# Kernel tuning notes

Hardware: AMD Instinct MI355X
Metric: run time of the kernel (lower is better)

## Reference

```python
import jax, jax.numpy as jnp
import numpy as np

NUM_CLASSES = 10
EPS = 1e-6


def setup_inputs() -> dict:
    key = jax.random.key(0)
    kx, ky, k1, k2, k3, k4 = jax.random.split(key, 6)
    B, N, F = 64, 4096, 256
    hidden, out_dim = 64, 128
    return {
        "X_support": jax.random.normal(kx, (B, N, F), dtype=jnp.float32),
        "y_support": jax.random.randint(ky, (B, N), 0, NUM_CLASSES, dtype=jnp.int64),
        "W1": jax.random.normal(k1, (6, hidden), dtype=jnp.float32) * 0.4,
        "b1": jax.random.normal(k2, (hidden,), dtype=jnp.float32) * 0.02,
        "W2": jax.random.normal(k3, (hidden, out_dim), dtype=jnp.float32) * 0.12,
        "b2": jax.random.normal(k4, (out_dim,), dtype=jnp.float32) * 0.02,
    }


def _stats(X, y):
    # X: [B, N, F] float, y: [B, N] int labels in [0, NUM_CLASSES)
    B, N, F = X.shape
    missing_rate = jnp.isnan(X).astype(jnp.float32).mean(axis=1)        # [B, F]
    cleaned = jnp.nan_to_num(X, nan=0.0)                                # [B, N, F]

    # unique ratio per column: count distinct via sorted adjacent diffs
    srt = jnp.sort(cleaned, axis=1)
    uniq = 1.0 + (jnp.diff(srt, axis=1) != 0).astype(jnp.float32).sum(axis=1)  # [B, F]
    unique_ratio = uniq / max(1, N)

    mean = cleaned.mean(axis=1)                                         # [B, F]
    variance = cleaned.var(axis=1)                                      # [B, F] (unbiased=False)
    mean_abs = jnp.abs(cleaned).mean(axis=1)
    max_abs = jnp.abs(cleaned).max(axis=1)

    # classification target score: between-class variance / overall variance
    onehot = jax.nn.one_hot(y, NUM_CLASSES, dtype=jnp.float32)          # [B, N, C]
    counts = onehot.sum(axis=1)                                         # [B, C]
    class_sums = jnp.einsum("bnc,bnf->bcf", onehot, cleaned)            # [B, C, F]
    class_means = class_sums / jnp.maximum(counts, 1.0)[:, :, None]     # [B, C, F] (0 for empty class)
    dev2 = jnp.square(class_means - mean[:, None, :])                   # [B, C, F]
    between_var = jnp.einsum("bc,bcf->bf", counts, dev2) / jnp.maximum(counts.sum(axis=1), 1.0)[:, None]
    overall_var = jnp.maximum(variance, EPS)
    target_score = between_var / overall_var                            # [B, F]

    stats = jnp.stack(
        [target_score, missing_rate, unique_ratio, variance, mean_abs, max_abs], axis=-1
    )  # [B, F, 6]
    return jnp.nan_to_num(stats, nan=0.0, posinf=0.0, neginf=0.0)


def reference(X_support, y_support, W1, b1, W2, b2):
    stats = _stats(X_support, y_support)                                # [B, F, 6]
    h = jax.nn.gelu(stats @ W1 + b1, approximate=False)
    return h @ W2 + b2                                                  # [B, F, output_dim]
```

## Files before the change

### kernel.cpp

```cpp
#include <hip/hip_runtime.h>
#include <math.h>

#define NB 64
#define NN 4096
#define NF 256
#define NC 10
#define NSPLIT 16
#define CH 256
#define LW 263
#define EMPTYK 0xFFFFFFFFu

__global__ void k_counts(const int* __restrict__ Y, int* __restrict__ counts) {
  __shared__ int hist[NC];
  const int b = blockIdx.x;
  if (threadIdx.x < NC) hist[threadIdx.x] = 0;
  __syncthreads();
  for (int i = threadIdx.x; i < NN; i += blockDim.x) {
    int c = Y[b * NN + i];
    if (c >= 0 && c < NC) atomicAdd(&hist[c], 1);
  }
  __syncthreads();
  if (threadIdx.x < NC) counts[b * NC + threadIdx.x] = hist[threadIdx.x];
}

__global__ __launch_bounds__(256) void k_stats(const float* __restrict__ X,
                                               const int* __restrict__ Y,
                                               unsigned* __restrict__ XT,
                                               float* __restrict__ P) {
  __shared__ unsigned ldsT[32 * LW];
  const int bi = blockIdx.x;
  const int b = bi >> 4, sp = bi & 15;
  const int t = threadIdx.x;
  const int w = t >> 6, l = t & 63;
  const int n0 = sp * CH;
  const float4* Xv = (const float4*)X;

  float s1[4] = {0, 0, 0, 0}, s2[4] = {0, 0, 0, 0}, sab[4] = {0, 0, 0, 0};
  float mab[4] = {0, 0, 0, 0}, nanc[4] = {0, 0, 0, 0};
  float cls[NC][4] = {};
  const int colbase = 4 * l + (l >> 3);

#define ADD4(c) do { cls[c][0]+=cv[0]; cls[c][1]+=cv[1]; cls[c][2]+=cv[2]; cls[c][3]+=cv[3]; } while(0)

  for (int tile = 0; tile < CH / 32; ++tile) {
#pragma unroll 4
    for (int it = 0; it < 8; ++it) {
      const int r = it * 4 + w;
      const int n = n0 + tile * 32 + r;
      float4 v4 = Xv[(size_t)(b * NN + n) * (NF / 4) + l];
      float v[4] = {v4.x, v4.y, v4.z, v4.w};
      float cv[4];
      unsigned ub[4];
#pragma unroll
      for (int q = 0; q < 4; ++q) {
        float c = v[q];
        if (c != c) { nanc[q] += 1.f; c = 0.f; }
        cv[q] = c;
        s1[q] += c;
        s2[q] = fmaf(c, c, s2[q]);
        float a = fabsf(c);
        sab[q] += a;
        mab[q] = fmaxf(mab[q], a);
        ub[q] = (c == 0.f) ? 0u : __float_as_uint(c);
      }
      const int ys = __builtin_amdgcn_readfirstlane(Y[b * NN + n]);
      switch (ys) {
        case 0: ADD4(0); break; case 1: ADD4(1); break;
        case 2: ADD4(2); break; case 3: ADD4(3); break;
        case 4: ADD4(4); break; case 5: ADD4(5); break;
        case 6: ADD4(6); break; case 7: ADD4(7); break;
        case 8: ADD4(8); break; case 9: ADD4(9); break;
        default: break;
      }
      const int lb = r * LW + colbase;
      ldsT[lb + 0] = ub[0]; ldsT[lb + 1] = ub[1];
      ldsT[lb + 2] = ub[2]; ldsT[lb + 3] = ub[3];
    }
    __syncthreads();
#pragma unroll
    for (int j = 0; j < 8; ++j) {
      const int idx = t + 256 * j;
      const int f = idx >> 3, rr4 = idx & 7;
      const int fo = f + (f >> 5);
      uint4 o;
      o.x = ldsT[(rr4 * 4 + 0) * LW + fo];
      o.y = ldsT[(rr4 * 4 + 1) * LW + fo];
      o.z = ldsT[(rr4 * 4 + 2) * LW + fo];
      o.w = ldsT[(rr4 * 4 + 3) * LW + fo];
      ((uint4*)(XT + (size_t)(b * NF + f) * NN + n0 + tile * 32))[rr4] = o;
    }
    __syncthreads();
  }

  float* red = (float*)ldsT;
  for (int ph = 0; ph < 4; ++ph) {
    if (w == ph) {
#pragma unroll
      for (int ff = 0; ff < 4; ++ff) {
        const int f = 4 * l + ff;
        float vals[16];
        vals[0] = s1[ff]; vals[1] = s2[ff]; vals[2] = sab[ff];
        vals[3] = mab[ff]; vals[4] = nanc[ff];
#pragma unroll
        for (int c = 0; c < NC; ++c) vals[5 + c] = cls[c][ff];
        vals[15] = 0.f;
        if (ph == 0) {
#pragma unroll
          for (int s = 0; s < 16; ++s) red[f * 16 + s] = vals[s];
        } else {
          red[f * 16 + 0] += vals[0];
          red[f * 16 + 1] += vals[1];
          red[f * 16 + 2] += vals[2];
          red[f * 16 + 3] = fmaxf(red[f * 16 + 3], vals[3]);
          red[f * 16 + 4] += vals[4];
#pragma unroll
          for (int c = 0; c < NC; ++c) red[f * 16 + 5 + c] += vals[5 + c];
        }
      }
    }
    __syncthreads();
  }
  float4* Pv = (float4*)(P + ((size_t)(b * NSPLIT + sp) * NF + t) * 16);
  const float4* rv = (const float4*)(red + t * 16);
  Pv[0] = rv[0]; Pv[1] = rv[1]; Pv[2] = rv[2]; Pv[3] = rv[3];
#undef ADD4
}

__global__ __launch_bounds__(256) void k_uniq(const unsigned* __restrict__ XT,
                                              unsigned* __restrict__ uniq) {
  __shared__ unsigned tab[8192];
  const int t = threadIdx.x;
  const size_t base = (size_t)blockIdx.x * NN;

  const uint4* Xv = (const uint4*)(XT + base);
  uint4 kv0 = Xv[t], kv1 = Xv[256 + t], kv2 = Xv[512 + t], kv3 = Xv[768 + t];

  uint4* tv = (uint4*)tab;
  const uint4 e4 = make_uint4(EMPTYK, EMPTYK, EMPTYK, EMPTYK);
#pragma unroll
  for (int i = 0; i < 8; ++i) tv[t + 256 * i] = e4;

  unsigned key[16] = {kv0.x, kv0.y, kv0.z, kv0.w, kv1.x, kv1.y, kv1.z, kv1.w,
                      kv2.x, kv2.y, kv2.z, kv2.w, kv3.x, kv3.y, kv3.z, kv3.w};
  unsigned h[16];
#pragma unroll
  for (int q = 0; q < 16; ++q) h[q] = (key[q] * 2654435761u) >> 19;
  unsigned pend = 0xFFFFu;
  unsigned salt = 0x9E3779B9u;
  int cnt = 0;
  __syncthreads();

  while (true) {
#pragma unroll
    for (int q = 0; q < 16; ++q)
      if (pend & (1u << q)) tab[h[q]] = key[q];
    __syncthreads();
#pragma unroll
    for (int q = 0; q < 16; ++q)
      if (pend & (1u << q)) {
        if (tab[h[q]] == key[q]) pend &= ~(1u << q);
        else h[q] = ((key[q] ^ salt) * 2654435761u) >> 19;
      }
    salt += 0x9E3779B9u;
    __syncthreads();
#pragma unroll
    for (int i = 0; i < 8; ++i) {
      uint4 v = tv[t + 256 * i];
      cnt += (v.x != EMPTYK) + (v.y != EMPTYK) + (v.z != EMPTYK) + (v.w != EMPTYK);
      tv[t + 256 * i] = e4;
    }
    if (__syncthreads_count(pend != 0) == 0) break;
  }

  for (int off = 32; off; off >>= 1) cnt += __shfl_down(cnt, off, 64);
  __syncthreads();
  if ((t & 63) == 0) tab[t >> 6] = (unsigned)cnt;
  __syncthreads();
  if (t == 0) uniq[blockIdx.x] = tab[0] + tab[1] + tab[2] + tab[3];
}

__global__ void k_finalize(const float* __restrict__ P, const int* __restrict__ counts,
                           const unsigned* __restrict__ uniq, float* __restrict__ stats6) {
  const int col = blockIdx.x * 256 + threadIdx.x;
  const int b = col >> 8;
  const int f = col & 255;
  float acc[16];
#pragma unroll
  for (int i = 0; i < 16; ++i) acc[i] = 0.f;
  for (int sp = 0; sp < NSPLIT; ++sp) {
    const float4* p4 = (const float4*)(P + ((size_t)(b * NSPLIT + sp) * NF + f) * 16);
    float4 A = p4[0], B4 = p4[1], C4 = p4[2], D4 = p4[3];
    acc[0] += A.x; acc[1] += A.y; acc[2] += A.z; acc[3] = fmaxf(acc[3], A.w);
    acc[4] += B4.x; acc[5] += B4.y; acc[6] += B4.z; acc[7] += B4.w;
    acc[8] += C4.x; acc[9] += C4.y; acc[10] += C4.z; acc[11] += C4.w;
    acc[12] += D4.x; acc[13] += D4.y; acc[14] += D4.z;
  }
  const float invN = 1.f / (float)NN;
  const float mean = acc[0] * invN;
  float var = acc[1] * invN - mean * mean;
  if (var < 0.f) var = 0.f;
  const float meanabs = acc[2] * invN;
  const float maxabs = acc[3];
  const float miss = acc[4] * invN;
  const float uratio = (float)uniq[col] * invN;
  float btw = 0.f;
#pragma unroll
  for (int c = 0; c < NC; ++c) {
    float cntc = (float)counts[b * NC + c];
    float m = acc[5 + c] / fmaxf(cntc, 1.f);
    float d = m - mean;
    btw = fmaf(cntc * d, d, btw);
  }
  btw *= invN;
  const float target = btw / fmaxf(var, 1e-6f);
  float st[6] = {target, miss, uratio, var, meanabs, maxabs};
#pragma unroll
  for (int i = 0; i < 6; ++i)
    if (!(fabsf(st[i]) <= 3.4028235e38f)) st[i] = 0.f;
#pragma unroll
  for (int i = 0; i < 6; ++i) stats6[(size_t)col * 6 + i] = st[i];
}

__global__ __launch_bounds__(256) void k_mlp(const float* __restrict__ stats6,
                                             const float* __restrict__ W1,
                                             const float* __restrict__ b1,
                                             const float* __restrict__ W2,
                                             const float* __restrict__ b2,
                                             float* __restrict__ out) {
  __shared__ float w1s[6 * 64];
  __shared__ float b1s[64];
  __shared__ float w2s[64 * 128];
  __shared__ float b2s[128];
  __shared__ float sts[32 * 6];
  __shared__ float hs[64 * 36];
  const int t = threadIdx.x;
  const int cb0 = blockIdx.x * 32;
  for (int i = t; i < 96; i += 256) ((float4*)w1s)[i] = ((const float4*)W1)[i];
  if (t < 64) b1s[t] = b1[t];
  for (int i = t; i < 2048; i += 256) ((float4*)w2s)[i] = ((const float4*)W2)[i];
  if (t < 128) b2s[t] = b2[t];
  if (t < 48) ((float4*)sts)[t] = ((const float4*)(stats6 + (size_t)cb0 * 6))[t];
  __syncthreads();

  const int k = t & 63, cg = t >> 6;
#pragma unroll
  for (int cc = 0; cc < 8; ++cc) {
    const int col = cg + 4 * cc;
    float pre = b1s[k];
#pragma unroll
    for (int s = 0; s < 6; ++s) pre = fmaf(sts[col * 6 + s], w1s[s * 64 + k], pre);
    const float h = 0.5f * pre * (1.f + erff(pre * 0.70710678118654752f));
    hs[k * 36 + col] = h;
  }
  __syncthreads();

  const int j4 = (t & 31) * 4, c4 = (t >> 5) * 4;
  float4 a[4];
  const float4 bj = *(const float4*)&b2s[j4];
  a[0] = bj; a[1] = bj; a[2] = bj; a[3] = bj;
  for (int kk = 0; kk < 64; ++kk) {
    const float4 wv = *(const float4*)&w2s[kk * 128 + j4];
    const float4 hv = *(const float4*)&hs[kk * 36 + c4];
    const float hc[4] = {hv.x, hv.y, hv.z, hv.w};
#pragma unroll
    for (int ci = 0; ci < 4; ++ci) {
      a[ci].x = fmaf(hc[ci], wv.x, a[ci].x);
      a[ci].y = fmaf(hc[ci], wv.y, a[ci].y);
      a[ci].z = fmaf(hc[ci], wv.z, a[ci].z);
      a[ci].w = fmaf(hc[ci], wv.w, a[ci].w);
    }
  }
#pragma unroll
  for (int ci = 0; ci < 4; ++ci) {
    const int col = cb0 + c4 + ci;
    *(float4*)&out[(size_t)col * 128 + j4] = a[ci];
  }
}

extern "C" void kernel_launch(void* const* d_in, const int* in_sizes, int n_in,
                              void* d_out, int out_size, void* d_ws, size_t ws_size,
                              hipStream_t stream) {
  const float* X = (const float*)d_in[0];
  const int* Y = (const int*)d_in[1];
  const float* W1 = (const float*)d_in[2];
  const float* b1 = (const float*)d_in[3];
  const float* W2 = (const float*)d_in[4];
  const float* b2 = (const float*)d_in[5];
  float* out = (float*)d_out;

  char* w = (char*)d_ws;
  unsigned* XT = (unsigned*)w;
  float* P = (float*)(w + 268435456ull);
  float* stats6 = (float*)(w + 285212672ull);
  int* counts = (int*)(w + 285605888ull);
  unsigned* uniq = (unsigned*)(w + 285608448ull);

  k_counts<<<NB, 256, 0, stream>>>(Y, counts);
  k_stats<<<NB * NSPLIT, 256, 0, stream>>>(X, Y, XT, P);
  k_uniq<<<NB * NF, 256, 0, stream>>>(XT, uniq);
  k_finalize<<<64, 256, 0, stream>>>(P, counts, uniq, stats6);
  k_mlp<<<512, 256, 0, stream>>>(stats6, W1, b1, W2, b2, out);
}
```

Measured before the change: 654.2 us.

## Restructure stats kernel with register prefetch, per-column reduction, fused class counts

k_stats now prefetches the next 32-row tile into registers while the current tile is transposed. Each thread owns one column and accumulates moments and class sums by reading back the transposed LDS tile, which removes the four-phase cross-wave LDS reduction. The separate k_counts kernel is folded into k_finalize by computing the class histogram with wave shuffles. k_uniq merges one barrier with the termination count. The trade-offs are higher register pressure from the prefetch buffers and an extra LDS read pass per tile.

```diff
diff --git a/kernel.cpp b/kernel.cpp
--- a/kernel.cpp
+++ b/kernel.cpp
@@ -10,23 +10,10 @@
 #define LW 263
 #define EMPTYK 0xFFFFFFFFu
 
-__global__ void k_counts(const int* __restrict__ Y, int* __restrict__ counts) {
-  __shared__ int hist[NC];
-  const int b = blockIdx.x;
-  if (threadIdx.x < NC) hist[threadIdx.x] = 0;
-  __syncthreads();
-  for (int i = threadIdx.x; i < NN; i += blockDim.x) {
-    int c = Y[b * NN + i];
-    if (c >= 0 && c < NC) atomicAdd(&hist[c], 1);
-  }
-  __syncthreads();
-  if (threadIdx.x < NC) counts[b * NC + threadIdx.x] = hist[threadIdx.x];
-}
-
-__global__ __launch_bounds__(256) void k_stats(const float* __restrict__ X,
-                                               const int* __restrict__ Y,
-                                               unsigned* __restrict__ XT,
-                                               float* __restrict__ P) {
+__global__ __launch_bounds__(256, 4) void k_stats(const float* __restrict__ X,
+                                                  const int* __restrict__ Y,
+                                                  unsigned* __restrict__ XT,
+                                                  float* __restrict__ P) {
   __shared__ unsigned ldsT[32 * LW];
   const int bi = blockIdx.x;
   const int b = bi >> 4, sp = bi & 15;
@@ -35,48 +22,47 @@
   const int n0 = sp * CH;
   const float4* Xv = (const float4*)X;
 
-  float s1[4] = {0, 0, 0, 0}, s2[4] = {0, 0, 0, 0}, sab[4] = {0, 0, 0, 0};
-  float mab[4] = {0, 0, 0, 0}, nanc[4] = {0, 0, 0, 0};
-  float cls[NC][4] = {};
+  const int y0 = Y[b * NN + n0 + l];
+  const int y1 = Y[b * NN + n0 + 64 + l];
+  const int y2 = Y[b * NN + n0 + 128 + l];
+  const int y3 = Y[b * NN + n0 + 192 + l];
+
+  float s1 = 0.f, s2 = 0.f, sab = 0.f, mab = 0.f;
+  float cls[NC] = {};
+  float nanc4[4] = {0.f, 0.f, 0.f, 0.f};
+
   const int colbase = 4 * l + (l >> 3);
-
-#define ADD4(c) do { cls[c][0]+=cv[0]; cls[c][1]+=cv[1]; cls[c][2]+=cv[2]; cls[c][3]+=cv[3]; } while(0)
-
-  for (int tile = 0; tile < CH / 32; ++tile) {
-#pragma unroll 4
+  const int myoff = t + (t >> 5);
+
+  float4 pf[8];
+#pragma unroll
+  for (int it = 0; it < 8; ++it) {
+    const int n = n0 + it * 4 + w;
+    pf[it] = Xv[(size_t)(b * NN + n) * (NF / 4) + l];
+  }
+
+  for (int tile = 0; tile < 8; ++tile) {
+#pragma unroll
     for (int it = 0; it < 8; ++it) {
-      const int r = it * 4 + w;
-      const int n = n0 + tile * 32 + r;
-      float4 v4 = Xv[(size_t)(b * NN + n) * (NF / 4) + l];
-      float v[4] = {v4.x, v4.y, v4.z, v4.w};
-      float cv[4];
-      unsigned ub[4];
+      const float v[4] = {pf[it].x, pf[it].y, pf[it].z, pf[it].w};
+      const int lb = (it * 4 + w) * LW + colbase;
 #pragma unroll
       for (int q = 0; q < 4; ++q) {
         float c = v[q];
-        if (c != c) { nanc[q] += 1.f; c = 0.f; }
-        cv[q] = c;
-        s1[q] += c;
-        s2[q] = fmaf(c, c, s2[q]);
-        float a = fabsf(c);
-        sab[q] += a;
-        mab[q] = fmaxf(mab[q], a);
-        ub[q] = (c == 0.f) ? 0u : __float_as_uint(c);
+        if (c != c) { nanc4[q] += 1.f; c = 0.f; }
+        ldsT[lb + q] = (c == 0.f) ? 0u : __float_as_uint(c);
       }
-      const int ys = __builtin_amdgcn_readfirstlane(Y[b * NN + n]);
-      switch (ys) {
-        case 0: ADD4(0); break; case 1: ADD4(1); break;
-        case 2: ADD4(2); break; case 3: ADD4(3); break;
-        case 4: ADD4(4); break; case 5: ADD4(5); break;
-        case 6: ADD4(6); break; case 7: ADD4(7); break;
-        case 8: ADD4(8); break; case 9: ADD4(9); break;
-        default: break;
+    }
+    __syncthreads();
+
+    if (tile < 7) {
+#pragma unroll
+      for (int it = 0; it < 8; ++it) {
+        const int n = n0 + (tile + 1) * 32 + it * 4 + w;
+        pf[it] = Xv[(size_t)(b * NN + n) * (NF / 4) + l];
       }
-      const int lb = r * LW + colbase;
-      ldsT[lb + 0] = ub[0]; ldsT[lb + 1] = ub[1];
-      ldsT[lb + 2] = ub[2]; ldsT[lb + 3] = ub[3];
-    }
-    __syncthreads();
+    }
+
 #pragma unroll
     for (int j = 0; j < 8; ++j) {
       const int idx = t + 256 * j;
@@ -89,41 +75,47 @@
       o.w = ldsT[(rr4 * 4 + 3) * LW + fo];
       ((uint4*)(XT + (size_t)(b * NF + f) * NN + n0 + tile * 32))[rr4] = o;
     }
+
+    const int kk = tile >> 1;
+    const int yl = (kk & 2) ? ((kk & 1) ? y3 : y2) : ((kk & 1) ? y1 : y0);
+    const int lbase = (tile & 1) * 32;
+#pragma unroll
+    for (int r = 0; r < 32; ++r) {
+      const float c = __uint_as_float(ldsT[r * LW + myoff]);
+      const int y = __builtin_amdgcn_readlane(yl, lbase + r);
+      s1 += c;
+      s2 = fmaf(c, c, s2);
+      const float a = fabsf(c);
+      sab += a;
+      mab = fmaxf(mab, a);
+      switch (y) {
+        case 0: cls[0] += c; break; case 1: cls[1] += c; break;
+        case 2: cls[2] += c; break; case 3: cls[3] += c; break;
+        case 4: cls[4] += c; break; case 5: cls[5] += c; break;
+        case 6: cls[6] += c; break; case 7: cls[7] += c; break;
+        case 8: cls[8] += c; break; case 9: cls[9] += c; break;
+        default: break;
+      }
+    }
     __syncthreads();
   }
 
-  float* red = (float*)ldsT;
-  for (int ph = 0; ph < 4; ++ph) {
-    if (w == ph) {
-#pragma unroll
-      for (int ff = 0; ff < 4; ++ff) {
-        const int f = 4 * l + ff;
-        float vals[16];
-        vals[0] = s1[ff]; vals[1] = s2[ff]; vals[2] = sab[ff];
-        vals[3] = mab[ff]; vals[4] = nanc[ff];
-#pragma unroll
-        for (int c = 0; c < NC; ++c) vals[5 + c] = cls[c][ff];
-        vals[15] = 0.f;
-        if (ph == 0) {
-#pragma unroll
-          for (int s = 0; s < 16; ++s) red[f * 16 + s] = vals[s];
-        } else {
-          red[f * 16 + 0] += vals[0];
-          red[f * 16 + 1] += vals[1];
-          red[f * 16 + 2] += vals[2];
-          red[f * 16 + 3] = fmaxf(red[f * 16 + 3], vals[3]);
-          red[f * 16 + 4] += vals[4];
-#pragma unroll
-          for (int c = 0; c < NC; ++c) red[f * 16 + 5 + c] += vals[5 + c];
-        }
-      }
-    }
-    __syncthreads();
-  }
+  float* nl = (float*)ldsT;
+#pragma unroll
+  for (int q = 0; q < 4; ++q) nl[w * 256 + 4 * l + q] = nanc4[q];
+  __syncthreads();
+  const float nanc = nl[t] + nl[256 + t] + nl[512 + t] + nl[768 + t];
+
+  float vals[16];
+  vals[0] = s1; vals[1] = s2; vals[2] = sab; vals[3] = mab; vals[4] = nanc;
+#pragma unroll
+  for (int c = 0; c < NC; ++c) vals[5 + c] = cls[c];
+  vals[15] = 0.f;
   float4* Pv = (float4*)(P + ((size_t)(b * NSPLIT + sp) * NF + t) * 16);
-  const float4* rv = (const float4*)(red + t * 16);
-  Pv[0] = rv[0]; Pv[1] = rv[1]; Pv[2] = rv[2]; Pv[3] = rv[3];
-#undef ADD4
+  Pv[0] = *(float4*)&vals[0];
+  Pv[1] = *(float4*)&vals[4];
+  Pv[2] = *(float4*)&vals[8];
+  Pv[3] = *(float4*)&vals[12];
 }
 
 __global__ __launch_bounds__(256) void k_uniq(const unsigned* __restrict__ XT,
@@ -162,14 +154,15 @@
         else h[q] = ((key[q] ^ salt) * 2654435761u) >> 19;
       }
     salt += 0x9E3779B9u;
-    __syncthreads();
+    const int live = __syncthreads_count(pend != 0);
 #pragma unroll
     for (int i = 0; i < 8; ++i) {
       uint4 v = tv[t + 256 * i];
       cnt += (v.x != EMPTYK) + (v.y != EMPTYK) + (v.z != EMPTYK) + (v.w != EMPTYK);
-      tv[t + 256 * i] = e4;
-    }
-    if (__syncthreads_count(pend != 0) == 0) break;
+      if (live) tv[t + 256 * i] = e4;
+    }
+    if (!live) break;
+    __syncthreads();
   }
 
   for (int off = 32; off; off >>= 1) cnt += __shfl_down(cnt, off, 64);
@@ -179,11 +172,37 @@
   if (t == 0) uniq[blockIdx.x] = tab[0] + tab[1] + tab[2] + tab[3];
 }
 
-__global__ void k_finalize(const float* __restrict__ P, const int* __restrict__ counts,
-                           const unsigned* __restrict__ uniq, float* __restrict__ stats6) {
-  const int col = blockIdx.x * 256 + threadIdx.x;
-  const int b = col >> 8;
-  const int f = col & 255;
+__global__ __launch_bounds__(256) void k_finalize(const float* __restrict__ P,
+                                                  const int* __restrict__ Y,
+                                                  const unsigned* __restrict__ uniq,
+                                                  float* __restrict__ stats6) {
+  __shared__ float whist[4 * NC];
+  const int b = blockIdx.x;
+  const int t = threadIdx.x;
+
+  int cnt[NC];
+#pragma unroll
+  for (int c = 0; c < NC; ++c) cnt[c] = 0;
+#pragma unroll
+  for (int i = 0; i < 16; ++i) {
+    const int y = Y[b * NN + 256 * i + t];
+#pragma unroll
+    for (int c = 0; c < NC; ++c) cnt[c] += (y == c) ? 1 : 0;
+  }
+#pragma unroll
+  for (int c = 0; c < NC; ++c) {
+    int v = cnt[c];
+    for (int off = 32; off; off >>= 1) v += __shfl_down(v, off, 64);
+    cnt[c] = v;
+  }
+  if ((t & 63) == 0) {
+#pragma unroll
+    for (int c = 0; c < NC; ++c) whist[(t >> 6) * NC + c] = (float)cnt[c];
+  }
+  __syncthreads();
+
+  const int f = t;
+  const int col = b * 256 + f;
   float acc[16];
 #pragma unroll
   for (int i = 0; i < 16; ++i) acc[i] = 0.f;
@@ -206,9 +225,9 @@
   float btw = 0.f;
 #pragma unroll
   for (int c = 0; c < NC; ++c) {
-    float cntc = (float)counts[b * NC + c];
-    float m = acc[5 + c] / fmaxf(cntc, 1.f);
-    float d = m - mean;
+    const float cntc = whist[c] + whist[NC + c] + whist[2 * NC + c] + whist[3 * NC + c];
+    const float m = acc[5 + c] / fmaxf(cntc, 1.f);
+    const float d = m - mean;
     btw = fmaf(cntc * d, d, btw);
   }
   btw *= invN;
@@ -292,12 +311,10 @@
   unsigned* XT = (unsigned*)w;
   float* P = (float*)(w + 268435456ull);
   float* stats6 = (float*)(w + 285212672ull);
-  int* counts = (int*)(w + 285605888ull);
   unsigned* uniq = (unsigned*)(w + 285608448ull);
 
-  k_counts<<<NB, 256, 0, stream>>>(Y, counts);
   k_stats<<<NB * NSPLIT, 256, 0, stream>>>(X, Y, XT, P);
   k_uniq<<<NB * NF, 256, 0, stream>>>(XT, uniq);
-  k_finalize<<<64, 256, 0, stream>>>(P, counts, uniq, stats6);
+  k_finalize<<<NB, 256, 0, stream>>>(P, Y, uniq, stats6);
   k_mlp<<<512, 256, 0, stream>>>(stats6, W1, b1, W2, b2, out);
 }
```

Result: faster. 596.8 us (-8.8%).
